# Optimization experiments

Measured on AMD Instinct MI355X. Metric: run time of the kernel, lower is better.

The kernel has to match this reference:

```python
import jax, jax.numpy as jnp
import numpy as np
from jax import lax

B_J0 = 0.01   # config.b_j0
R_M = 1.0     # config.R_m
BETA = 1.8    # isAdapt=1 branch
GAMMA = 0.5   # config.gamma
LENS = 0.5    # config.lens
SCALE = 6.0   # config.scale
HIGHT = 0.15  # config.hight


def _gauss(x, mu, sigma):
    return jnp.exp(-(x - mu) ** 2 / (2.0 * sigma ** 2)) / jnp.sqrt(2.0 * jnp.pi) / sigma


@jax.custom_vjp
def spike_fn(x):
    return (x > 0).astype(x.dtype)

def _spike_fwd(x):
    return spike_fn(x), x

def _spike_bwd(x, g):
    # 'MG' multi-gaussian surrogate gradient from ActFun_adp.backward
    temp = (_gauss(x, 0.0, LENS) * (1.0 + HIGHT)
            - _gauss(x, LENS, SCALE * LENS) * HIGHT
            - _gauss(x, -LENS, SCALE * LENS) * HIGHT)
    return (g * temp * GAMMA,)

spike_fn.defvjp(_spike_fwd, _spike_bwd)


def setup_inputs() -> dict:
    key = jax.random.key(0)
    ks = jax.random.split(key, 20)
    B, T, I, H, O = 256, 250, 700, 128, 20
    def xav(k, shape):
        lim = jnp.sqrt(6.0 / (shape[0] + shape[1]))
        return jax.random.uniform(k, shape, jnp.float32, -lim, lim)
    def orth(k, n):
        a = jax.random.normal(k, (n, n), jnp.float32)
        q, r = jnp.linalg.qr(a)
        return q * jnp.sign(jnp.diag(r))[None, :]
    return {
        'input': jax.random.normal(ks[0], (B, T, I), jnp.float32),
        'A1_mask': jnp.ones((H, H), jnp.float32),
        'A2_mask': jnp.ones((H, H), jnp.float32),
        'W_ih1': xav(ks[1], (H, I)), 'b_ih1': jnp.zeros((H,), jnp.float32),
        'W_h1h1': orth(ks[2], H), 'b_h1h1': jnp.zeros((H,), jnp.float32),
        'W_h1h2': xav(ks[3], (H, H)), 'b_h1h2': jnp.zeros((H,), jnp.float32),
        'W_h2h2': orth(ks[4], H), 'b_h2h2': jnp.zeros((H,), jnp.float32),
        'W_h2o': xav(ks[5], (O, H)), 'b_h2o': jnp.zeros((O,), jnp.float32),
        'tau_adp_h1': 150.0 + 10.0 * jax.random.normal(ks[6], (H,), jnp.float32),
        'tau_adp_h2': 150.0 + 10.0 * jax.random.normal(ks[7], (H,), jnp.float32),
        'tau_m_h1': 20.0 + 5.0 * jax.random.normal(ks[8], (H,), jnp.float32),
        'tau_m_h2': 20.0 + 5.0 * jax.random.normal(ks[9], (H,), jnp.float32),
        'tau_m_o': 20.0 + 5.0 * jax.random.normal(ks[10], (O,), jnp.float32),
        'hid1_mem0': jax.random.uniform(ks[11], (B, H), jnp.float32),
        'hid2_mem0': jax.random.uniform(ks[12], (B, H), jnp.float32),
        'out_mem0': jax.random.uniform(ks[13], (B, O), jnp.float32),
    }


def reference(input, A1_mask, A2_mask,
              W_ih1, b_ih1, W_h1h1, b_h1h1, W_h1h2, b_h1h2,
              W_h2h2, b_h2h2, W_h2o, b_h2o,
              tau_adp_h1, tau_adp_h2, tau_m_h1, tau_m_h2, tau_m_o,
              hid1_mem0, hid2_mem0, out_mem0):
    B, T, _ = input.shape
    H = W_ih1.shape[0]
    O = W_h2o.shape[0]
    # time-constant decays (dt = 1), computed once
    a1 = jnp.exp(-1.0 / tau_m_h1)
    r1 = jnp.exp(-1.0 / tau_adp_h1)
    a2 = jnp.exp(-1.0 / tau_m_h2)
    r2 = jnp.exp(-1.0 / tau_adp_h2)
    ao = jnp.exp(-1.0 / tau_m_o)

    xT = jnp.swapaxes(input, 0, 1)  # [T, B, I]
    carry0 = (hid1_mem0, jnp.zeros((B, H), input.dtype), jnp.full((B, H), B_J0, input.dtype),
              hid2_mem0, jnp.zeros((B, H), input.dtype), jnp.full((B, H), B_J0, input.dtype),
              out_mem0, jnp.zeros((B, O), input.dtype))

    def step(carry, xs):
        x_t, t = xs
        h1m, h1s, b1, h2m, h2s, b2, om, acc = carry
        # layer 1: input + recurrent drive, adaptive threshold LIF update
        in1 = x_t @ W_ih1.T + b_ih1 + h1s @ W_h1h1.T + b_h1h1
        b1 = r1 * b1 + (1.0 - r1) * h1s
        Bth1 = B_J0 + BETA * b1
        h1m = h1m * a1 + (1.0 - a1) * R_M * in1 - Bth1 * h1s
        h1s = spike_fn(h1m - Bth1)
        # layer 2
        in2 = h1s @ W_h1h2.T + b_h1h2 + h2s @ W_h2h2.T + b_h2h2
        b2 = r2 * b2 + (1.0 - r2) * h2s
        Bth2 = B_J0 + BETA * b2
        h2m = h2m * a2 + (1.0 - a2) * R_M * in2 - Bth2 * h2s
        h2s = spike_fn(h2m - Bth2)
        # leaky-integrator readout (no spike)
        om = om * ao + (1.0 - ao) * R_M * (h2s @ W_h2o.T + b_h2o)
        # accumulate softmax only for t > 10
        acc = acc + jnp.where(t > 10, 1.0, 0.0) * jax.nn.softmax(om, axis=1)
        return (h1m, h1s, b1, h2m, h2s, b2, om, acc), None

    final, _ = lax.scan(step, carry0, (xT, jnp.arange(T)))
    output = final[-1]
    A_norm = jnp.sum(jnp.abs(W_h1h1)) + jnp.sum(jnp.abs(W_h2h2))
    return output, A_norm


if __name__ == '__main__':
    out = reference(**setup_inputs())
    print(out[0].shape, out[1])
```

## Files before the change

kernel.cpp:

```cpp
#include <hip/hip_runtime.h>
#include <hip/hip_bf16.h>
#include <stdint.h>

#define HN 128
#define TSTEPS 250
#define ON 20
#define GK 700
#define NKT 22

typedef _Float16 h2 __attribute__((ext_vector_type(2)));
typedef _Float16 h8 __attribute__((ext_vector_type(8)));
typedef float f4 __attribute__((ext_vector_type(4)));

__device__ __forceinline__ uint32_t pack2u(float x, float y) {
    h2 p; p.x = (_Float16)x; p.y = (_Float16)y;
    return __builtin_bit_cast(uint32_t, p);
}

__global__ __launch_bounds__(256) void ff_gemm(const float* __restrict__ X,
                                               const float* __restrict__ W,
                                               const float* __restrict__ bias,
                                               float* __restrict__ out) {
    __shared__ __align__(16) uint32_t Xs[2][128][16];
    __shared__ __align__(16) uint32_t Ws[2][128][16];
    const int tid   = threadIdx.x;
    const int w     = tid >> 6;
    const int lane  = tid & 63;
    const int m0    = blockIdx.x * 128;
    const int srow  = tid & 127;
    const int shalf = tid >> 7;
    const int lr    = lane & 15;
    const int lg    = lane >> 4;

    f4 acc[2][8];
#pragma unroll
    for (int m = 0; m < 2; ++m)
#pragma unroll
        for (int n = 0; n < 8; ++n) acc[m][n] = (f4){0.f, 0.f, 0.f, 0.f};

    float4 x4[4], w4[4];

#define LOADT(t)                                                               \
    {                                                                          \
        const int k0 = (t) * 32 + shalf * 16;                                  \
        if ((t) < 21 || shalf == 0) {                                          \
            _Pragma("unroll")                                                  \
            for (int q = 0; q < 4; ++q) {                                      \
                x4[q] = *(const float4*)&X[(size_t)(m0 + srow) * GK + k0 + q * 4]; \
                w4[q] = *(const float4*)&W[(size_t)srow * GK + k0 + q * 4];    \
            }                                                                  \
        } else {                                                               \
            _Pragma("unroll")                                                  \
            for (int q = 0; q < 3; ++q) {                                      \
                x4[q] = *(const float4*)&X[(size_t)(m0 + srow) * GK + k0 + q * 4]; \
                w4[q] = *(const float4*)&W[(size_t)srow * GK + k0 + q * 4];    \
            }                                                                  \
            x4[3] = (float4){0.f, 0.f, 0.f, 0.f};                              \
            w4[3] = (float4){0.f, 0.f, 0.f, 0.f};                              \
        }                                                                      \
    }
#define STORET(buf)                                                            \
    {                                                                          \
        _Pragma("unroll")                                                      \
        for (int q = 0; q < 4; ++q) {                                          \
            Xs[buf][srow][shalf * 8 + 2 * q]     = pack2u(x4[q].x, x4[q].y);   \
            Xs[buf][srow][shalf * 8 + 2 * q + 1] = pack2u(x4[q].z, x4[q].w);   \
            Ws[buf][srow][shalf * 8 + 2 * q]     = pack2u(w4[q].x, w4[q].y);   \
            Ws[buf][srow][shalf * 8 + 2 * q + 1] = pack2u(w4[q].z, w4[q].w);   \
        }                                                                      \
    }

    LOADT(0);
    STORET(0);
    __syncthreads();
    int cur = 0;
    for (int t = 0; t < NKT; ++t) {
        if (t + 1 < NKT) LOADT(t + 1);
        h8 a[2];
#pragma unroll
        for (int m = 0; m < 2; ++m) {
            const uint4 au = *(const uint4*)&Xs[cur][w * 32 + m * 16 + lr][lg * 4];
            a[m] = __builtin_bit_cast(h8, au);
        }
#pragma unroll
        for (int n = 0; n < 8; ++n) {
            const uint4 bu = *(const uint4*)&Ws[cur][n * 16 + lr][lg * 4];
            const h8 bf = __builtin_bit_cast(h8, bu);
            acc[0][n] = __builtin_amdgcn_mfma_f32_16x16x32_f16(a[0], bf, acc[0][n], 0, 0, 0);
            acc[1][n] = __builtin_amdgcn_mfma_f32_16x16x32_f16(a[1], bf, acc[1][n], 0, 0, 0);
        }
        if (t + 1 < NKT) STORET(cur ^ 1);
        __syncthreads();
        cur ^= 1;
    }

    float bv[8];
#pragma unroll
    for (int n = 0; n < 8; ++n) bv[n] = bias[n * 16 + lr];
#pragma unroll
    for (int m = 0; m < 2; ++m)
#pragma unroll
        for (int q = 0; q < 4; ++q) {
            const size_t row = (size_t)(m0 + w * 32 + m * 16 + lg * 4 + q);
#pragma unroll
            for (int n = 0; n < 8; ++n)
                out[row * HN + n * 16 + lr] = acc[m][n][q] + bv[n];
        }
#undef LOADT
#undef STORET
}

__device__ __forceinline__ int mvq(const uint4 (&W)[8][HN],
                                   const uint4 (&sv)[8], int j) {
    int a = 0;
#pragma unroll
    for (int g = 0; g < 8; ++g) {
        const uint4 wq = W[g][j];
        const uint4 sq = sv[g];
        a = __builtin_amdgcn_sdot4((int)wq.x, (int)sq.x, a, false);
        a = __builtin_amdgcn_sdot4((int)wq.y, (int)sq.y, a, false);
        a = __builtin_amdgcn_sdot4((int)wq.z, (int)sq.z, a, false);
        a = __builtin_amdgcn_sdot4((int)wq.w, (int)sq.w, a, false);
    }
    return a;
}
__device__ __forceinline__ int mvqo(const uint4 (&W)[8][32],
                                    const uint4 (&sv)[8], int j) {
    int a = 0;
#pragma unroll
    for (int g = 0; g < 8; ++g) {
        const uint4 wq = W[g][j];
        const uint4 sq = sv[g];
        a = __builtin_amdgcn_sdot4((int)wq.x, (int)sq.x, a, false);
        a = __builtin_amdgcn_sdot4((int)wq.y, (int)sq.y, a, false);
        a = __builtin_amdgcn_sdot4((int)wq.z, (int)sq.z, a, false);
        a = __builtin_amdgcn_sdot4((int)wq.w, (int)sq.w, a, false);
    }
    return a;
}

#define LOADQ(arr, buf, sv)                                                    \
    {                                                                          \
        const uint4* _p = (const uint4*)&arr[buf][0];                          \
        _Pragma("unroll") for (int _g = 0; _g < 8; ++_g) sv[_g] = _p[_g];      \
    }

__global__ __launch_bounds__(512) void srnn_pipe9(
    const float* __restrict__ ff,
    const float* __restrict__ W_h1h1, const float* __restrict__ b_h1h1,
    const float* __restrict__ W_h1h2, const float* __restrict__ b_h1h2,
    const float* __restrict__ W_h2h2, const float* __restrict__ b_h2h2,
    const float* __restrict__ W_h2o,  const float* __restrict__ b_h2o,
    const float* __restrict__ tau_adp_h1, const float* __restrict__ tau_adp_h2,
    const float* __restrict__ tau_m_h1,   const float* __restrict__ tau_m_h2,
    const float* __restrict__ tau_m_o,
    const float* __restrict__ h1m0, const float* __restrict__ h2m0,
    const float* __restrict__ om0,
    float* __restrict__ out) {
    const int b    = blockIdx.x;
    const int tid  = threadIdx.x;
    const int w    = tid >> 6;
    const int lane = tid & 63;

    __shared__ __align__(16) uint4 WQA[8][HN];
    __shared__ __align__(16) uint4 WQB[8][HN];
    __shared__ __align__(16) uint4 WQC[8][HN];
    __shared__ __align__(16) uint4 WQO[8][32];
    __shared__ float scA[HN], scB[HN], scC[HN], scO[32];
    __shared__ __align__(16) uint32_t s1w[2][32];
    __shared__ __align__(16) uint32_t s2w[2][32];
    __shared__ float pBbuf[2][HN];
    __shared__ float rdot_lds[2][32];

    if (tid < 416) {
        const int role = tid >> 7;
        const int j    = tid & 127;
        const bool isO = (role == 3);
        const bool on  = !isO || (j < 32);
        if (on) {
            const float* src = nullptr;
            bool valid = true;
            if (!isO) {
                src = (role == 0 ? W_h1h1 : role == 1 ? W_h1h2 : W_h2h2) + j * HN;
            } else if (j < ON) {
                src = W_h2o + j * HN;
            } else {
                valid = false;
            }
            float amax = 0.f;
            if (valid) {
#pragma unroll
                for (int q = 0; q < 32; ++q) {
                    float4 v = *(const float4*)&src[q * 4];
                    amax = fmaxf(amax, fmaxf(fmaxf(fabsf(v.x), fabsf(v.y)),
                                             fmaxf(fabsf(v.z), fabsf(v.w))));
                }
            }
            const float qs = (valid && amax > 0.f) ? 127.f / amax : 0.f;
#pragma unroll
            for (int g = 0; g < 8; ++g) {
                uint32_t u[4] = {0u, 0u, 0u, 0u};
                if (valid) {
#pragma unroll
                    for (int e = 0; e < 4; ++e) {
                        float4 v = *(const float4*)&src[g * 16 + e * 4];
                        const int q0 = (int)rintf(v.x * qs), q1 = (int)rintf(v.y * qs);
                        const int q2 = (int)rintf(v.z * qs), q3 = (int)rintf(v.w * qs);
                        u[e] = (uint32_t)(q0 & 255) | ((uint32_t)(q1 & 255) << 8) |
                               ((uint32_t)(q2 & 255) << 16) | ((uint32_t)(q3 & 255) << 24);
                    }
                }
                uint4 w4; w4.x = u[0]; w4.y = u[1]; w4.z = u[2]; w4.w = u[3];
                if (isO) WQO[g][j] = w4;
                else if (role == 0) WQA[g][j] = w4;
                else if (role == 1) WQB[g][j] = w4;
                else WQC[g][j] = w4;
            }
            const float os = (valid && amax > 0.f) ? amax / 127.f : 0.f;
            if (isO) scO[j] = os;
            else if (role == 0) scA[j] = os;
            else if (role == 1) scB[j] = os;
            else scC[j] = os;
        }
    }
    if (tid < 32) {
        s1w[0][tid] = 0u; s1w[1][tid] = 0u;
        s2w[0][tid] = 0u; s2w[1][tid] = 0u;
    }
    __syncthreads();

    if (w < 2) {
        const int j = (w << 6) + lane;
        const float sA = scA[j];
        float h1m = h1m0[b * HN + j];
        const float a1 = expf(-1.f / tau_m_h1[j]);
        const float r1 = expf(-1.f / tau_adp_h1[j]);
        const float bi = b_h1h1[j];
        float b1 = 0.01f, s1p = 0.f;
        const float* fp = ff + (size_t)b * TSTEPS * HN + j;
        float fc = fp[0], fn = fp[HN];
        for (int i = 0; i < TSTEPS + 4; ++i) {
            if (i < TSTEPS) {
                const float f2 = (i + 2 < TSTEPS) ? fp[(size_t)(i + 2) * HN] : 0.f;
                uint4 sv[8];
                LOADQ(s1w, (i + 1) & 1, sv);
                const float pA = sA * (float)mvq(WQA, sv, j);
                b1 = r1 * b1 + (1.f - r1) * s1p;
                const float Bt = 0.01f + 1.8f * b1;
                h1m = h1m * a1 + (1.f - a1) * (fc + bi + pA) - Bt * s1p;
                const int sp = (h1m - Bt > 0.f) ? 1 : 0;
                s1p = (float)sp;
                int pk = sp | (__shfl_down(sp, 1) << 8) |
                         (__shfl_down(sp, 2) << 16) | (__shfl_down(sp, 3) << 24);
                if ((lane & 3) == 0) s1w[i & 1][(w << 4) + (lane >> 2)] = (uint32_t)pk;
                fc = fn; fn = f2;
            }
            __syncthreads();
        }
    } else if (w < 4) {
        const int j = ((w - 2) << 6) + lane;
        const float sB = scB[j];
        for (int i = 0; i < TSTEPS + 4; ++i) {
            if (i >= 1 && i <= TSTEPS) {
                uint4 sv[8];
                LOADQ(s1w, (i - 1) & 1, sv);
                pBbuf[(i - 1) & 1][j] = sB * (float)mvq(WQB, sv, j);
            }
            __syncthreads();
        }
    } else if (w < 6) {
        const int j = ((w - 4) << 6) + lane;
        const float sC = scC[j];
        float h2m = h2m0[b * HN + j];
        const float a2 = expf(-1.f / tau_m_h2[j]);
        const float r2 = expf(-1.f / tau_adp_h2[j]);
        const float bi = b_h1h2[j] + b_h2h2[j];
        float b2v = 0.01f, s2p = 0.f;
        for (int i = 0; i < TSTEPS + 4; ++i) {
            if (i >= 2 && i <= TSTEPS + 1) {
                const int k2 = i - 2;
                uint4 sv[8];
                LOADQ(s2w, (k2 + 1) & 1, sv);
                const float pC = sC * (float)mvq(WQC, sv, j);
                const float in2 = pBbuf[k2 & 1][j] + pC + bi;
                b2v = r2 * b2v + (1.f - r2) * s2p;
                const float Bt = 0.01f + 1.8f * b2v;
                h2m = h2m * a2 + (1.f - a2) * in2 - Bt * s2p;
                const int sp = (h2m - Bt > 0.f) ? 1 : 0;
                s2p = (float)sp;
                int pk = sp | (__shfl_down(sp, 1) << 8) |
                         (__shfl_down(sp, 2) << 16) | (__shfl_down(sp, 3) << 24);
                if ((lane & 3) == 0) s2w[k2 & 1][((w - 4) << 4) + (lane >> 2)] = (uint32_t)pk;
            }
            __syncthreads();
        }
    } else if (w == 6) {
        const int o = lane;
        const float sO = (o < 32) ? scO[o] : 0.f;
        for (int i = 0; i < TSTEPS + 4; ++i) {
            if (i >= 3 && i <= TSTEPS + 2 && o < ON) {
                const int k3 = i - 3;
                uint4 sv[8];
                LOADQ(s2w, k3 & 1, sv);
                rdot_lds[k3 & 1][o] = sO * (float)mvqo(WQO, sv, o);
            }
            __syncthreads();
        }
    } else {
        const int o = lane;
        float om = 0.f, ao = 0.f, bo = 0.f, acc = 0.f;
        if (o < ON) {
            om = om0[b * ON + o];
            ao = expf(-1.f / tau_m_o[o]);
            bo = b_h2o[o];
        }
        for (int i = 0; i < TSTEPS + 4; ++i) {
            if (i >= 4) {
                const int k4 = i - 4;
                if (o < ON)
                    om = om * ao + (1.f - ao) * (rdot_lds[k4 & 1][o] + bo);
                float mx = (o < ON) ? om : -3.4e38f;
#pragma unroll
                for (int m = 16; m >= 1; m >>= 1)
                    mx = fmaxf(mx, __shfl_xor(mx, m));
                float e = (o < ON) ? __expf(om - mx) : 0.f;
                float den = e;
#pragma unroll
                for (int m = 16; m >= 1; m >>= 1)
                    den += __shfl_xor(den, m);
                if (o < ON && k4 > 10) acc += e / den;
            }
            __syncthreads();
        }
        if (o < ON) out[b * ON + o] = acc;
    }
}

__global__ void anorm_kernel(const float* __restrict__ W1,
                             const float* __restrict__ W2,
                             float* __restrict__ out) {
    __shared__ float red[256];
    float s = 0.f;
    for (int i = threadIdx.x; i < HN * HN; i += 256)
        s += fabsf(W1[i]) + fabsf(W2[i]);
    red[threadIdx.x] = s;
    __syncthreads();
    for (int off = 128; off > 0; off >>= 1) {
        if (threadIdx.x < off) red[threadIdx.x] += red[threadIdx.x + off];
        __syncthreads();
    }
    if (threadIdx.x == 0) out[256 * ON] = red[0];
}

extern "C" void kernel_launch(void* const* d_in, const int* in_sizes, int n_in,
                              void* d_out, int out_size, void* d_ws, size_t ws_size,
                              hipStream_t stream) {
    const float* input      = (const float*)d_in[0];
    const float* W_ih1      = (const float*)d_in[3];
    const float* b_ih1      = (const float*)d_in[4];
    const float* W_h1h1     = (const float*)d_in[5];
    const float* b_h1h1     = (const float*)d_in[6];
    const float* W_h1h2     = (const float*)d_in[7];
    const float* b_h1h2     = (const float*)d_in[8];
    const float* W_h2h2     = (const float*)d_in[9];
    const float* b_h2h2     = (const float*)d_in[10];
    const float* W_h2o      = (const float*)d_in[11];
    const float* b_h2o      = (const float*)d_in[12];
    const float* tau_adp_h1 = (const float*)d_in[13];
    const float* tau_adp_h2 = (const float*)d_in[14];
    const float* tau_m_h1   = (const float*)d_in[15];
    const float* tau_m_h2   = (const float*)d_in[16];
    const float* tau_m_o    = (const float*)d_in[17];
    const float* h1m0       = (const float*)d_in[18];
    const float* h2m0       = (const float*)d_in[19];
    const float* om0        = (const float*)d_in[20];

    float* out   = (float*)d_out;
    float* ffbuf = (float*)d_ws;

    anorm_kernel<<<1, 256, 0, stream>>>(W_h1h1, W_h2h2, out);
    ff_gemm<<<500, 256, 0, stream>>>(input, W_ih1, b_ih1, ffbuf);
    srnn_pipe9<<<256, 512, 0, stream>>>(ffbuf, W_h1h1, b_h1h1, W_h1h2, b_h1h2,
                                        W_h2h2, b_h2h2, W_h2o, b_h2o,
                                        tau_adp_h1, tau_adp_h2,
                                        tau_m_h1, tau_m_h2, tau_m_o,
                                        h1m0, h2m0, om0, out);
}
```

Measured before the change: 221.8 us.

## Shorten per-step critical path: ballot spike packing, split dot chains, serial softmax

Packs spike bits with a single wave ballot plus a multiply-mask nibble-to-byte expansion, replacing three cross-lane shuffles per step in both spiking layers. Splits each int8 dot-product accumulation into four independent chains to cut dependent latency. Rewrites the readout wave so every lane computes all 20 softmax outputs serially from vectorised LDS reads, avoiding cross-lane reductions. All three target the latency of each barrier-synchronised pipeline step, at the cost of redundant per-lane work and more registers in the readout wave.

```diff
diff --git a/kernel.cpp b/kernel.cpp
--- a/kernel.cpp
+++ b/kernel.cpp
@@ -112,31 +112,31 @@
 
 __device__ __forceinline__ int mvq(const uint4 (&W)[8][HN],
                                    const uint4 (&sv)[8], int j) {
-    int a = 0;
+    int a0 = 0, a1 = 0, a2 = 0, a3 = 0;
 #pragma unroll
     for (int g = 0; g < 8; ++g) {
         const uint4 wq = W[g][j];
         const uint4 sq = sv[g];
-        a = __builtin_amdgcn_sdot4((int)wq.x, (int)sq.x, a, false);
-        a = __builtin_amdgcn_sdot4((int)wq.y, (int)sq.y, a, false);
-        a = __builtin_amdgcn_sdot4((int)wq.z, (int)sq.z, a, false);
-        a = __builtin_amdgcn_sdot4((int)wq.w, (int)sq.w, a, false);
-    }
-    return a;
+        a0 = __builtin_amdgcn_sdot4((int)wq.x, (int)sq.x, a0, false);
+        a1 = __builtin_amdgcn_sdot4((int)wq.y, (int)sq.y, a1, false);
+        a2 = __builtin_amdgcn_sdot4((int)wq.z, (int)sq.z, a2, false);
+        a3 = __builtin_amdgcn_sdot4((int)wq.w, (int)sq.w, a3, false);
+    }
+    return (a0 + a1) + (a2 + a3);
 }
 __device__ __forceinline__ int mvqo(const uint4 (&W)[8][32],
                                     const uint4 (&sv)[8], int j) {
-    int a = 0;
+    int a0 = 0, a1 = 0, a2 = 0, a3 = 0;
 #pragma unroll
     for (int g = 0; g < 8; ++g) {
         const uint4 wq = W[g][j];
         const uint4 sq = sv[g];
-        a = __builtin_amdgcn_sdot4((int)wq.x, (int)sq.x, a, false);
-        a = __builtin_amdgcn_sdot4((int)wq.y, (int)sq.y, a, false);
-        a = __builtin_amdgcn_sdot4((int)wq.z, (int)sq.z, a, false);
-        a = __builtin_amdgcn_sdot4((int)wq.w, (int)sq.w, a, false);
-    }
-    return a;
+        a0 = __builtin_amdgcn_sdot4((int)wq.x, (int)sq.x, a0, false);
+        a1 = __builtin_amdgcn_sdot4((int)wq.y, (int)sq.y, a1, false);
+        a2 = __builtin_amdgcn_sdot4((int)wq.z, (int)sq.z, a2, false);
+        a3 = __builtin_amdgcn_sdot4((int)wq.w, (int)sq.w, a3, false);
+    }
+    return (a0 + a1) + (a2 + a3);
 }
 
 #define LOADQ(arr, buf, sv)                                                    \
@@ -145,7 +145,11 @@
         _Pragma("unroll") for (int _g = 0; _g < 8; ++_g) sv[_g] = _p[_g];      \
     }
 
-__global__ __launch_bounds__(512) void srnn_pipe9(
+__device__ __forceinline__ uint32_t nib2bytes(uint32_t nib) {
+    return ((nib & 15u) * 0x00204081u) & 0x01010101u;
+}
+
+__global__ __launch_bounds__(512) void srnn_pipe10(
     const float* __restrict__ ff,
     const float* __restrict__ W_h1h1, const float* __restrict__ b_h1h1,
     const float* __restrict__ W_h1h2, const float* __restrict__ b_h1h2,
@@ -170,7 +174,7 @@
     __shared__ __align__(16) uint32_t s1w[2][32];
     __shared__ __align__(16) uint32_t s2w[2][32];
     __shared__ float pBbuf[2][HN];
-    __shared__ float rdot_lds[2][32];
+    __shared__ __align__(16) float rdot_lds[2][32];
 
     if (tid < 416) {
         const int role = tid >> 7;
@@ -250,9 +254,12 @@
                 h1m = h1m * a1 + (1.f - a1) * (fc + bi + pA) - Bt * s1p;
                 const int sp = (h1m - Bt > 0.f) ? 1 : 0;
                 s1p = (float)sp;
-                int pk = sp | (__shfl_down(sp, 1) << 8) |
-                         (__shfl_down(sp, 2) << 16) | (__shfl_down(sp, 3) << 24);
-                if ((lane & 3) == 0) s1w[i & 1][(w << 4) + (lane >> 2)] = (uint32_t)pk;
+                const unsigned long long mk = __ballot(sp);
+                const uint32_t mlo = (uint32_t)mk, mhi = (uint32_t)(mk >> 32);
+                if (lane < 16) {
+                    const uint32_t nib = (lane < 8 ? mlo : mhi) >> ((lane & 7) * 4);
+                    s1w[i & 1][(w << 4) + lane] = nib2bytes(nib);
+                }
                 fc = fn; fn = f2;
             }
             __syncthreads();
@@ -288,9 +295,12 @@
                 h2m = h2m * a2 + (1.f - a2) * in2 - Bt * s2p;
                 const int sp = (h2m - Bt > 0.f) ? 1 : 0;
                 s2p = (float)sp;
-                int pk = sp | (__shfl_down(sp, 1) << 8) |
-                         (__shfl_down(sp, 2) << 16) | (__shfl_down(sp, 3) << 24);
-                if ((lane & 3) == 0) s2w[k2 & 1][((w - 4) << 4) + (lane >> 2)] = (uint32_t)pk;
+                const unsigned long long mk = __ballot(sp);
+                const uint32_t mlo = (uint32_t)mk, mhi = (uint32_t)(mk >> 32);
+                if (lane < 16) {
+                    const uint32_t nib = (lane < 8 ? mlo : mhi) >> ((lane & 7) * 4);
+                    s2w[k2 & 1][((w - 4) << 4) + lane] = nib2bytes(nib);
+                }
             }
             __syncthreads();
         }
@@ -307,32 +317,60 @@
             __syncthreads();
         }
     } else {
-        const int o = lane;
-        float om = 0.f, ao = 0.f, bo = 0.f, acc = 0.f;
-        if (o < ON) {
-            om = om0[b * ON + o];
-            ao = expf(-1.f / tau_m_o[o]);
-            bo = b_h2o[o];
+        float omv[ON], accv[ON], aov[ON], bov[ON];
+#pragma unroll
+        for (int k = 0; k < ON; ++k) {
+            omv[k]  = om0[b * ON + k];
+            aov[k]  = expf(-1.f / tau_m_o[k]);
+            bov[k]  = b_h2o[k];
+            accv[k] = 0.f;
         }
         for (int i = 0; i < TSTEPS + 4; ++i) {
             if (i >= 4) {
                 const int k4 = i - 4;
-                if (o < ON)
-                    om = om * ao + (1.f - ao) * (rdot_lds[k4 & 1][o] + bo);
-                float mx = (o < ON) ? om : -3.4e38f;
-#pragma unroll
-                for (int m = 16; m >= 1; m >>= 1)
-                    mx = fmaxf(mx, __shfl_xor(mx, m));
-                float e = (o < ON) ? __expf(om - mx) : 0.f;
-                float den = e;
-#pragma unroll
-                for (int m = 16; m >= 1; m >>= 1)
-                    den += __shfl_xor(den, m);
-                if (o < ON && k4 > 10) acc += e / den;
+                const float4* rp = (const float4*)&rdot_lds[k4 & 1][0];
+                const float4 r0 = rp[0], r1 = rp[1], r2 = rp[2], r3 = rp[3], r4 = rp[4];
+                float rd[ON];
+                rd[0] = r0.x;  rd[1] = r0.y;  rd[2] = r0.z;  rd[3] = r0.w;
+                rd[4] = r1.x;  rd[5] = r1.y;  rd[6] = r1.z;  rd[7] = r1.w;
+                rd[8] = r2.x;  rd[9] = r2.y;  rd[10] = r2.z; rd[11] = r2.w;
+                rd[12] = r3.x; rd[13] = r3.y; rd[14] = r3.z; rd[15] = r3.w;
+                rd[16] = r4.x; rd[17] = r4.y; rd[18] = r4.z; rd[19] = r4.w;
+#pragma unroll
+                for (int k = 0; k < ON; ++k)
+                    omv[k] = omv[k] * aov[k] + (1.f - aov[k]) * (rd[k] + bov[k]);
+                float m0 = omv[0], m1 = omv[1], m2 = omv[2], m3 = omv[3];
+#pragma unroll
+                for (int k = 4; k < ON; k += 4) {
+                    m0 = fmaxf(m0, omv[k]);
+                    m1 = fmaxf(m1, omv[k + 1]);
+                    m2 = fmaxf(m2, omv[k + 2]);
+                    m3 = fmaxf(m3, omv[k + 3]);
+                }
+                const float mx = fmaxf(fmaxf(m0, m1), fmaxf(m2, m3));
+                float e[ON];
+                float d0 = 0.f, d1 = 0.f, d2 = 0.f, d3 = 0.f;
+#pragma unroll
+                for (int k = 0; k < ON; k += 4) {
+                    e[k]     = __expf(omv[k] - mx);     d0 += e[k];
+                    e[k + 1] = __expf(omv[k + 1] - mx); d1 += e[k + 1];
+                    e[k + 2] = __expf(omv[k + 2] - mx); d2 += e[k + 2];
+                    e[k + 3] = __expf(omv[k + 3] - mx); d3 += e[k + 3];
+                }
+                const float den = (d0 + d1) + (d2 + d3);
+                if (k4 > 10) {
+                    const float rden = 1.f / den;
+#pragma unroll
+                    for (int k = 0; k < ON; ++k)
+                        accv[k] = fmaf(e[k], rden, accv[k]);
+                }
             }
             __syncthreads();
         }
-        if (o < ON) out[b * ON + o] = acc;
+        if (lane == 0) {
+#pragma unroll
+            for (int k = 0; k < ON; ++k) out[b * ON + k] = accv[k];
+        }
     }
 }
 
@@ -380,9 +418,9 @@
 
     anorm_kernel<<<1, 256, 0, stream>>>(W_h1h1, W_h2h2, out);
     ff_gemm<<<500, 256, 0, stream>>>(input, W_ih1, b_ih1, ffbuf);
-    srnn_pipe9<<<256, 512, 0, stream>>>(ffbuf, W_h1h1, b_h1h1, W_h1h2, b_h1h2,
-                                        W_h2h2, b_h2h2, W_h2o, b_h2o,
-                                        tau_adp_h1, tau_adp_h2,
-                                        tau_m_h1, tau_m_h2, tau_m_o,
-                                        h1m0, h2m0, om0, out);
-}
+    srnn_pipe10<<<256, 512, 0, stream>>>(ffbuf, W_h1h1, b_h1h1, W_h1h2, b_h1h2,
+                                         W_h2h2, b_h2h2, W_h2o, b_h2o,
+                                         tau_adp_h1, tau_adp_h2,
+                                         tau_m_h1, tau_m_h2, tau_m_o,
+                                         h1m0, h2m0, om0, out);
+}
```

Result: slower. 229.8 us (+3.6%).
